# Kernel tuning notes

Measured on AMD Instinct MI355X. Metric: run time of the kernel, lower is better.

## Reference

```python
import jax, jax.numpy as jnp
import numpy as np

B, S, D, H = 2, 2048, 1024, 16
HD = D // H  # head_dim = 64


def setup_inputs() -> dict:
    key = jax.random.key(0)
    ks = jax.random.split(key, 5)
    scale = 1.0 / np.sqrt(D)
    return {
        "x": jax.random.normal(ks[0], (B, S, D), dtype=jnp.float32),
        "w_q": jax.random.normal(ks[1], (D, D), dtype=jnp.float32) * scale,
        "b_q": jnp.zeros((D,), dtype=jnp.float32),
        "w_k": jax.random.normal(ks[2], (D, D), dtype=jnp.float32) * scale,
        "b_k": jnp.zeros((D,), dtype=jnp.float32),
        "w_v": jax.random.normal(ks[3], (D, D), dtype=jnp.float32) * scale,
        "b_v": jnp.zeros((D,), dtype=jnp.float32),
        "w_out": jax.random.normal(ks[4], (D, D), dtype=jnp.float32) * scale,
        "b_out": jnp.zeros((D,), dtype=jnp.float32),
    }


def reference(x, w_q, b_q, w_k, b_k, w_v, b_v, w_out, b_out):
    # Linear projections (torch Linear: x @ W.T + b)
    q = x @ w_q.T + b_q
    k = x @ w_k.T + b_k
    v = x @ w_v.T + b_v
    # split heads: [B, S, D] -> [B, H, S, HD]
    split = lambda t: t.reshape(B, S, H, HD).transpose(0, 2, 1, 3)
    q, k, v = split(q), split(k), split(v)
    # scaled dot-product attention with causal (tril) mask
    scores = jnp.einsum("bhqd,bhkd->bhqk", q, k) / jnp.sqrt(jnp.float32(HD))
    causal = jnp.tril(jnp.ones((S, S), dtype=bool))  # mask from causal_masking_function
    scores = jnp.where(causal, scores, jnp.float32(-1e9))
    probs = jax.nn.softmax(scores, axis=-1)
    # dropout(0.1) is identity in eval mode
    out = jnp.einsum("bhqk,bhkd->bhqd", probs, v)
    out = out.transpose(0, 2, 1, 3).reshape(B, S, D)
    return out @ w_out.T + b_out
```

## Files before the change

### kernel.cpp

```cpp
#include <hip/hip_runtime.h>

typedef __attribute__((ext_vector_type(8))) short bf16x8;
typedef __attribute__((ext_vector_type(4))) float f32x4;

__device__ __forceinline__ unsigned short f2b(float f) {
    unsigned u = __builtin_bit_cast(unsigned, f);
    u += 0x7fffu + ((u >> 16) & 1u);
    return (unsigned short)(u >> 16);
}

#define GLD_LDS(gp, lp) __builtin_amdgcn_global_load_lds( \
    (const __attribute__((address_space(1))) void*)(gp),  \
    (__attribute__((address_space(3))) void*)(lp), 16, 0, 0)

#define MFMA16(a, b, cacc) __builtin_amdgcn_mfma_f32_16x16x32_bf16(a, b, cacc, 0, 0, 0)

#define QSCL 0.18033688011112042f

__global__ __launch_bounds__(256) void cvt_all(const float* __restrict__ x,
        const float* __restrict__ w0, const float* __restrict__ w1,
        const float* __restrict__ w2, const float* __restrict__ w3,
        short* xb, short* o0, short* o1, short* o2, short* o3) {
    int i = blockIdx.x * 256 + threadIdx.x;
    const float* in; short* out; int off; float scl = 1.0f;
    if (i < (1 << 20)) { in = x; out = xb; off = i; }
    else {
        int j = (i - (1 << 20)) >> 18;
        off = (i - (1 << 20)) & ((1 << 18) - 1);
        switch (j) {
            case 0: in = w0; out = o0; scl = QSCL; break;
            case 1: in = w1; out = o1; break;
            case 2: in = w2; out = o2; break;
            default: in = w3; out = o3; break;
        }
    }
    float4 v = reinterpret_cast<const float4*>(in)[off];
    short4 o;
    o.x = (short)f2b(v.x * scl); o.y = (short)f2b(v.y * scl);
    o.z = (short)f2b(v.z * scl); o.w = (short)f2b(v.w * scl);
    reinterpret_cast<short4*>(out)[off] = o;
}

__global__ __launch_bounds__(256) void qkv_gemm(const short* __restrict__ A,
        const short* __restrict__ Wq, const short* __restrict__ Wk, const short* __restrict__ Wv,
        const float* __restrict__ bq, const float* __restrict__ bk, const float* __restrict__ bv,
        short* __restrict__ Oq, short* __restrict__ Ok, short* __restrict__ Ovt) {
    constexpr int Kd = 1024, N = 1024, S = 2048;
    __shared__ short As[2][128 * 32];
    __shared__ short Bs[2][128 * 32];
    const int mat = blockIdx.x >> 3;
    const int n0 = (blockIdx.x & 7) * 128, m0 = blockIdx.y * 128;
    const short* Bm = (mat == 0) ? Wq : (mat == 1 ? Wk : Wv);
    const float* bias = (mat == 0) ? bq : (mat == 1 ? bk : bv);
    const float bscl = (mat == 0) ? QSCL : 1.0f;
    const int t = threadIdx.x;
    const int w = t >> 6, lane = t & 63;
    const int wm = w >> 1, wn = w & 1;
    const int c = lane & 15, g = lane >> 4;

    f32x4 acc[4][4] = {};

    auto stage = [&](int buf, int k0) {
#pragma unroll
        for (int cc = 0; cc < 2; ++cc) {
            int e = (cc * 256 + t) * 8;
            int row = e >> 5;
            int col = (e & 31) ^ (((row >> 1) & 3) << 3);
            GLD_LDS(A + (size_t)(m0 + row) * Kd + k0 + col, &As[buf][e]);
            GLD_LDS(Bm + (size_t)(n0 + row) * Kd + k0 + col, &Bs[buf][e]);
        }
    };

    stage(0, 0);
    __syncthreads();
    int cur = 0;
    for (int ks = 0; ks < 32; ++ks) {
        if (ks + 1 < 32) stage(cur ^ 1, (ks + 1) * 32);
        const short* Ab_ = As[cur];
        const short* Bb_ = Bs[cur];
        bf16x8 af[4], bfr[4];
#pragma unroll
        for (int mi = 0; mi < 4; ++mi) {
            int ar = wm * 64 + mi * 16 + c;
            af[mi] = *(const bf16x8*)(Ab_ + ar * 32 + ((g * 8) ^ (((ar >> 1) & 3) << 3)));
        }
#pragma unroll
        for (int ni = 0; ni < 4; ++ni) {
            int br = wn * 64 + ni * 16 + c;
            bfr[ni] = *(const bf16x8*)(Bb_ + br * 32 + ((g * 8) ^ (((br >> 1) & 3) << 3)));
        }
#pragma unroll
        for (int mi = 0; mi < 4; ++mi)
#pragma unroll
            for (int ni = 0; ni < 4; ++ni)
                acc[mi][ni] = MFMA16(af[mi], bfr[ni], acc[mi][ni]);
        __syncthreads();
        cur ^= 1;
    }

    if (mat < 2) {
        short* Cb = (mat == 0) ? Oq : Ok;
#pragma unroll
        for (int mi = 0; mi < 4; ++mi)
#pragma unroll
            for (int ni = 0; ni < 4; ++ni) {
                int col = n0 + wn * 64 + ni * 16 + c;
                float bvv = bias[col] * bscl;
#pragma unroll
                for (int r = 0; r < 4; ++r) {
                    int row = m0 + wm * 64 + mi * 16 + g * 4 + r;
                    Cb[(size_t)row * N + col] = (short)f2b(acc[mi][ni][r] + bvv);
                }
            }
    } else {
#pragma unroll
        for (int mi = 0; mi < 4; ++mi)
#pragma unroll
            for (int ni = 0; ni < 4; ++ni) {
                int col = n0 + wn * 64 + ni * 16 + c;
                int h = col >> 6, hd = col & 63;
                float bvv = bias[col];
                int row0 = m0 + wm * 64 + mi * 16 + g * 4;
                int b = row0 >> 11, s = row0 & 2047;
                short4 pk;
                pk.x = (short)f2b(acc[mi][ni][0] + bvv);
                pk.y = (short)f2b(acc[mi][ni][1] + bvv);
                pk.z = (short)f2b(acc[mi][ni][2] + bvv);
                pk.w = (short)f2b(acc[mi][ni][3] + bvv);
                *(short4*)(Ovt + ((size_t)((b * 16 + h) * 64 + hd)) * S + s) = pk;
            }
    }
}

__global__ __launch_bounds__(256) void out_gemm(const short* __restrict__ A,
                                                const short* __restrict__ Bm,
                                                const float* __restrict__ bias,
                                                float* __restrict__ C) {
    constexpr int Kd = 1024, N = 1024;
    __shared__ short As[2][64 * 32];
    __shared__ short Bs[2][128 * 32];
    const int n0 = blockIdx.x * 128, m0 = blockIdx.y * 64;
    const int t = threadIdx.x;
    const int w = t >> 6, lane = t & 63;
    const int wm = w >> 1, wn = w & 1;
    const int c = lane & 15, g = lane >> 4;

    f32x4 acc[2][4] = {};

    auto stage = [&](int buf, int k0) {
        {
            int e = t * 8;
            int row = e >> 5;
            int col = (e & 31) ^ (((row >> 1) & 3) << 3);
            GLD_LDS(A + (size_t)(m0 + row) * Kd + k0 + col, &As[buf][e]);
        }
#pragma unroll
        for (int cc = 0; cc < 2; ++cc) {
            int e = (cc * 256 + t) * 8;
            int row = e >> 5;
            int col = (e & 31) ^ (((row >> 1) & 3) << 3);
            GLD_LDS(Bm + (size_t)(n0 + row) * Kd + k0 + col, &Bs[buf][e]);
        }
    };

    stage(0, 0);
    __syncthreads();
    int cur = 0;
    for (int ks = 0; ks < 32; ++ks) {
        if (ks + 1 < 32) stage(cur ^ 1, (ks + 1) * 32);
        const short* Ab_ = As[cur];
        const short* Bb_ = Bs[cur];
        bf16x8 af[2], bfr[4];
#pragma unroll
        for (int mi = 0; mi < 2; ++mi) {
            int ar = wm * 32 + mi * 16 + c;
            af[mi] = *(const bf16x8*)(Ab_ + ar * 32 + ((g * 8) ^ (((ar >> 1) & 3) << 3)));
        }
#pragma unroll
        for (int ni = 0; ni < 4; ++ni) {
            int br = wn * 64 + ni * 16 + c;
            bfr[ni] = *(const bf16x8*)(Bb_ + br * 32 + ((g * 8) ^ (((br >> 1) & 3) << 3)));
        }
#pragma unroll
        for (int mi = 0; mi < 2; ++mi)
#pragma unroll
            for (int ni = 0; ni < 4; ++ni)
                acc[mi][ni] = MFMA16(af[mi], bfr[ni], acc[mi][ni]);
        __syncthreads();
        cur ^= 1;
    }

#pragma unroll
    for (int mi = 0; mi < 2; ++mi)
#pragma unroll
        for (int ni = 0; ni < 4; ++ni) {
            int col = n0 + wn * 64 + ni * 16 + c;
            float bvv = bias[col];
#pragma unroll
            for (int r = 0; r < 4; ++r) {
                int row = m0 + wm * 32 + mi * 16 + g * 4 + r;
                C[(size_t)row * N + col] = acc[mi][ni][r] + bvv;
            }
        }
}

__global__ __launch_bounds__(256) void attn_kernel(const short* Q,
                                                   const short* __restrict__ Kg,
                                                   const short* __restrict__ Vt,
                                                   short* O) {
    constexpr int S = 2048, D = 1024;
    constexpr float M2 = 16.0f;
    __shared__ short Ks[64 * 64];
    __shared__ short Vs[64 * 64];
    __shared__ short Pl[4][16 * 64];
    const int id = blockIdx.x;
    const int bh = id & 31, b = bh >> 4, h = bh & 15;
    const int qtile = 31 - (id >> 5);
    const int t = threadIdx.x;
    const int w = t >> 6, lane = t & 63;
    const int c = lane & 15, g = lane >> 4;
    const int q0 = qtile * 64 + w * 16;

    const short* Qb = Q + (size_t)b * S * D + h * 64;
    const short* Kp = Kg + (size_t)b * S * D + h * 64;
    const short* Vp = Vt + (size_t)bh * 64 * S;

    bf16x8 aq0 = *(const bf16x8*)(Qb + (size_t)(q0 + c) * D + g * 8);
    bf16x8 aq1 = *(const bf16x8*)(Qb + (size_t)(q0 + c) * D + 32 + g * 8);

    f32x4 o[4] = {};
    float l_part[4] = {0.f, 0.f, 0.f, 0.f};

    const int ktmax = qtile + 1;
    for (int kt = 0; kt < ktmax; ++kt) {
        const int k0 = kt * 64;
#pragma unroll
        for (int cc = 0; cc < 2; ++cc) {
            int row = cc * 32 + (t >> 3);
            int colb = ((t & 7) * 16) ^ ((row & 7) << 4);
            GLD_LDS(Kp + (size_t)(k0 + row) * D + (colb >> 1), Ks + cc * 2048 + t * 8);
            GLD_LDS(Vp + (size_t)row * S + k0 + (colb >> 1), Vs + cc * 2048 + t * 8);
        }
        __syncthreads();

        f32x4 sc[4];
#pragma unroll
        for (int nt = 0; nt < 4; ++nt) {
            int row = nt * 16 + c;
            int sw = (row & 7) << 4;
            const char* rb = (const char*)Ks + row * 128;
            bf16x8 bk0 = *(const bf16x8*)(rb + ((g * 16) ^ sw));
            bf16x8 bk1 = *(const bf16x8*)(rb + ((64 + g * 16) ^ sw));
            f32x4 z = {};
            z = MFMA16(aq0, bk0, z);
            z = MFMA16(aq1, bk1, z);
            sc[nt] = z;
        }
        if (kt == ktmax - 1) {
#pragma unroll
            for (int nt = 0; nt < 4; ++nt)
#pragma unroll
                for (int r = 0; r < 4; ++r) {
                    int key = k0 + nt * 16 + c;
                    int qr = q0 + g * 4 + r;
                    if (key > qr) sc[nt][r] = -3e38f;
                }
        }
        char* pw = (char*)&Pl[w][0];
#pragma unroll
        for (int nt = 0; nt < 4; ++nt)
#pragma unroll
            for (int r = 0; r < 4; ++r) {
                float p = __builtin_exp2f(sc[nt][r] - M2);
                l_part[r] += p;
                int prow = g * 4 + r;
                int pb = ((nt * 16 + c) * 2) ^ ((prow & 7) << 4);
                *(short*)(pw + prow * 128 + pb) = (short)f2b(p);
            }
        asm volatile("" ::: "memory");
#pragma unroll
        for (int half = 0; half < 2; ++half) {
            bf16x8 pa = *(const bf16x8*)(pw + c * 128 + ((half * 64 + g * 16) ^ ((c & 7) << 4)));
#pragma unroll
            for (int n2 = 0; n2 < 4; ++n2) {
                int vrow = n2 * 16 + c;
                bf16x8 bv = *(const bf16x8*)((const char*)Vs + vrow * 128 +
                                             ((half * 64 + g * 16) ^ ((vrow & 7) << 4)));
                o[n2] = MFMA16(pa, bv, o[n2]);
            }
        }
        __syncthreads();
    }

#pragma unroll
    for (int d = 1; d < 16; d <<= 1)
#pragma unroll
        for (int r = 0; r < 4; ++r) l_part[r] += __shfl_xor(l_part[r], d);

    short* Ob = O + (size_t)b * S * D + h * 64;
#pragma unroll
    for (int r = 0; r < 4; ++r) {
        float inv = 1.0f / l_part[r];
        int row = q0 + g * 4 + r;
#pragma unroll
        for (int n2 = 0; n2 < 4; ++n2)
            Ob[(size_t)row * D + n2 * 16 + c] = (short)f2b(o[n2][r] * inv);
    }
}

extern "C" void kernel_launch(void* const* d_in, const int* in_sizes, int n_in,
                              void* d_out, int out_size, void* d_ws, size_t ws_size,
                              hipStream_t stream) {
    const float* x  = (const float*)d_in[0];
    const float* wq = (const float*)d_in[1];
    const float* bq = (const float*)d_in[2];
    const float* wk = (const float*)d_in[3];
    const float* bk = (const float*)d_in[4];
    const float* wv = (const float*)d_in[5];
    const float* bv = (const float*)d_in[6];
    const float* wo = (const float*)d_in[7];
    const float* bo = (const float*)d_in[8];
    float* out = (float*)d_out;

    char* ws = (char*)d_ws;
    const size_t SZ_X = (size_t)4096 * 1024 * 2;
    const size_t SZ_W = (size_t)1024 * 1024 * 2;
    short* xb  = (short*)(ws);
    short* wqb = (short*)(ws + SZ_X);
    short* wkb = (short*)(ws + SZ_X + SZ_W);
    short* wvb = (short*)(ws + SZ_X + 2 * SZ_W);
    short* wob = (short*)(ws + SZ_X + 3 * SZ_W);
    short* Qb  = (short*)(ws + SZ_X + 4 * SZ_W);
    short* Kbuf= (short*)(ws + 2 * SZ_X + 4 * SZ_W);
    short* Vtb = (short*)(ws + 3 * SZ_X + 4 * SZ_W);
    short* Ab  = Qb;

    cvt_all<<<8192, 256, 0, stream>>>(x, wq, wk, wv, wo, xb, wqb, wkb, wvb, wob);

    qkv_gemm<<<dim3(24, 32), 256, 0, stream>>>(xb, wqb, wkb, wvb, bq, bk, bv, Qb, Kbuf, Vtb);

    attn_kernel<<<1024, 256, 0, stream>>>(Qb, Kbuf, Vtb, Ab);

    out_gemm<<<dim3(8, 64), 256, 0, stream>>>(Ab, wob, bo, out);
}
```

Measured before the change: 209.3 us.

## Restructure QKV GEMM with 256x128 tiles, BK=64 and triple-buffered LDS pipeline

The QKV projection GEMM moves from 128x128 tiles with 256 threads to 256x128 tiles with 512 threads and a K step of 64. Staging goes from a double buffer to a three-deep ring in dynamic LDS (144 KiB), using a new XOR swizzle. Each iteration waits on vmcnt for the older stage, takes one barrier, and keeps two stages of global-to-LDS loads in flight. MFMA bursts run under raised wave priority. The aim is to hide global load latency, halve barriers per K, and reuse A across more columns. The cost is a large LDS footprint that allows only one block per CU, and 384 blocks for 256 CUs, which may leave the last wave of blocks unbalanced.

```diff
diff --git a/kernel.cpp b/kernel.cpp
--- a/kernel.cpp
+++ b/kernel.cpp
@@ -41,15 +41,19 @@
     reinterpret_cast<short4*>(out)[off] = o;
 }
 
-__global__ __launch_bounds__(256) void qkv_gemm(const short* __restrict__ A,
+__global__ __launch_bounds__(512) void qkv_gemm(const short* __restrict__ A,
         const short* __restrict__ Wq, const short* __restrict__ Wk, const short* __restrict__ Wv,
         const float* __restrict__ bq, const float* __restrict__ bk, const float* __restrict__ bv,
         short* __restrict__ Oq, short* __restrict__ Ok, short* __restrict__ Ovt) {
-    constexpr int Kd = 1024, N = 1024, S = 2048;
-    __shared__ short As[2][128 * 32];
-    __shared__ short Bs[2][128 * 32];
-    const int mat = blockIdx.x >> 3;
-    const int n0 = (blockIdx.x & 7) * 128, m0 = blockIdx.y * 128;
+    constexpr int Kd = 1024, S = 2048;
+    constexpr int ABUF = 256 * 64;
+    constexpr int BBUF = 128 * 64;
+    constexpr int TBUF = ABUF + BBUF;
+    extern __shared__ short lds[];
+    const int nt = blockIdx.x;
+    const int mat = nt >> 3;
+    const int n0m = (nt & 7) * 128;
+    const int m0 = blockIdx.y * 256;
     const short* Bm = (mat == 0) ? Wq : (mat == 1 ? Wk : Wv);
     const float* bias = (mat == 0) ? bq : (mat == 1 ? bk : bv);
     const float bscl = (mat == 0) ? QSCL : 1.0f;
@@ -61,41 +65,65 @@
     f32x4 acc[4][4] = {};
 
     auto stage = [&](int buf, int k0) {
+        short* La = lds + buf * TBUF;
+        short* Lb = La + ABUF;
+#pragma unroll
+        for (int cc = 0; cc < 4; ++cc) {
+            int chunk = cc * 512 + t;
+            int row = chunk >> 3, s = chunk & 7;
+            int colb = (s * 16) ^ ((row & 7) << 4);
+            GLD_LDS(A + (size_t)(m0 + row) * Kd + k0 + (colb >> 1), La + chunk * 8);
+        }
 #pragma unroll
         for (int cc = 0; cc < 2; ++cc) {
-            int e = (cc * 256 + t) * 8;
-            int row = e >> 5;
-            int col = (e & 31) ^ (((row >> 1) & 3) << 3);
-            GLD_LDS(A + (size_t)(m0 + row) * Kd + k0 + col, &As[buf][e]);
-            GLD_LDS(Bm + (size_t)(n0 + row) * Kd + k0 + col, &Bs[buf][e]);
+            int chunk = cc * 512 + t;
+            int row = chunk >> 3, s = chunk & 7;
+            int colb = (s * 16) ^ ((row & 7) << 4);
+            GLD_LDS(Bm + (size_t)(n0m + row) * Kd + k0 + (colb >> 1), Lb + chunk * 8);
         }
     };
 
     stage(0, 0);
-    __syncthreads();
+    stage(1, 64);
+
     int cur = 0;
-    for (int ks = 0; ks < 32; ++ks) {
-        if (ks + 1 < 32) stage(cur ^ 1, (ks + 1) * 32);
-        const short* Ab_ = As[cur];
-        const short* Bb_ = Bs[cur];
-        bf16x8 af[4], bfr[4];
-#pragma unroll
-        for (int mi = 0; mi < 4; ++mi) {
-            int ar = wm * 64 + mi * 16 + c;
-            af[mi] = *(const bf16x8*)(Ab_ + ar * 32 + ((g * 8) ^ (((ar >> 1) & 3) << 3)));
-        }
-#pragma unroll
-        for (int ni = 0; ni < 4; ++ni) {
-            int br = wn * 64 + ni * 16 + c;
-            bfr[ni] = *(const bf16x8*)(Bb_ + br * 32 + ((g * 8) ^ (((br >> 1) & 3) << 3)));
-        }
-#pragma unroll
-        for (int mi = 0; mi < 4; ++mi)
-#pragma unroll
-            for (int ni = 0; ni < 4; ++ni)
-                acc[mi][ni] = MFMA16(af[mi], bfr[ni], acc[mi][ni]);
-        __syncthreads();
-        cur ^= 1;
+#pragma unroll 1
+    for (int kt = 0; kt < 16; ++kt) {
+        if (kt < 15) asm volatile("s_waitcnt vmcnt(6)" ::: "memory");
+        else         asm volatile("s_waitcnt vmcnt(0)" ::: "memory");
+        __builtin_amdgcn_sched_barrier(0);
+        __builtin_amdgcn_s_barrier();
+        __builtin_amdgcn_sched_barrier(0);
+        if (kt + 2 < 16) {
+            int nbuf = cur + 2; if (nbuf >= 3) nbuf -= 3;
+            stage(nbuf, (kt + 2) * 64);
+        }
+        const short* La = lds + cur * TBUF;
+        const short* Lb = La + ABUF;
+#pragma unroll
+        for (int kk = 0; kk < 2; ++kk) {
+            bf16x8 af[4], bfr[4];
+#pragma unroll
+            for (int mi = 0; mi < 4; ++mi) {
+                int row = wm * 64 + mi * 16 + c;
+                af[mi] = *(const bf16x8*)((const char*)La + row * 128 +
+                                          ((kk * 64 + g * 16) ^ ((row & 7) << 4)));
+            }
+#pragma unroll
+            for (int ni = 0; ni < 4; ++ni) {
+                int row = wn * 64 + ni * 16 + c;
+                bfr[ni] = *(const bf16x8*)((const char*)Lb + row * 128 +
+                                           ((kk * 64 + g * 16) ^ ((row & 7) << 4)));
+            }
+            __builtin_amdgcn_s_setprio(1);
+#pragma unroll
+            for (int mi = 0; mi < 4; ++mi)
+#pragma unroll
+                for (int ni = 0; ni < 4; ++ni)
+                    acc[mi][ni] = MFMA16(af[mi], bfr[ni], acc[mi][ni]);
+            __builtin_amdgcn_s_setprio(0);
+        }
+        ++cur; if (cur == 3) cur = 0;
     }
 
     if (mat < 2) {
@@ -104,12 +132,12 @@
         for (int mi = 0; mi < 4; ++mi)
 #pragma unroll
             for (int ni = 0; ni < 4; ++ni) {
-                int col = n0 + wn * 64 + ni * 16 + c;
+                int col = n0m + wn * 64 + ni * 16 + c;
                 float bvv = bias[col] * bscl;
 #pragma unroll
                 for (int r = 0; r < 4; ++r) {
                     int row = m0 + wm * 64 + mi * 16 + g * 4 + r;
-                    Cb[(size_t)row * N + col] = (short)f2b(acc[mi][ni][r] + bvv);
+                    Cb[(size_t)row * 1024 + col] = (short)f2b(acc[mi][ni][r] + bvv);
                 }
             }
     } else {
@@ -117,7 +145,7 @@
         for (int mi = 0; mi < 4; ++mi)
 #pragma unroll
             for (int ni = 0; ni < 4; ++ni) {
-                int col = n0 + wn * 64 + ni * 16 + c;
+                int col = n0m + wn * 64 + ni * 16 + c;
                 int h = col >> 6, hd = col & 63;
                 float bvv = bias[col];
                 int row0 = m0 + wm * 64 + mi * 16 + g * 4;
@@ -335,9 +363,16 @@
     short* Vtb = (short*)(ws + 3 * SZ_X + 4 * SZ_W);
     short* Ab  = Qb;
 
+    static bool attr_set = false;
+    if (!attr_set) {
+        (void)hipFuncSetAttribute((const void*)qkv_gemm,
+                                  hipFuncAttributeMaxDynamicSharedMemorySize, 147456);
+        attr_set = true;
+    }
+
     cvt_all<<<8192, 256, 0, stream>>>(x, wq, wk, wv, wo, xb, wqb, wkb, wvb, wob);
 
-    qkv_gemm<<<dim3(24, 32), 256, 0, stream>>>(xb, wqb, wkb, wvb, bq, bk, bv, Qb, Kbuf, Vtb);
+    qkv_gemm<<<dim3(24, 16), 512, 147456, stream>>>(xb, wqb, wkb, wvb, bq, bk, bv, Qb, Kbuf, Vtb);
 
     attn_kernel<<<1024, 256, 0, stream>>>(Qb, Kbuf, Vtb, Ab);
 
```

Result: faster. 195.2 us (-6.7%).
